# Kernel optimization log

Hardware: AMD Instinct MI355X
Metric: run time of the kernel (lower is better)

Reference implementation:

```python
import jax, jax.numpy as jnp
import numpy as np

N_NODES = 100000
N_USERS = 50000
F_DIM = 256
H = 128
N_EDGES = 800000
BATCH = 4096
LN_EPS = 1e-5


def setup_inputs() -> dict:
    key = jax.random.key(0)
    ks = jax.random.split(key, 12)
    return {
        "node_features": jax.random.normal(ks[0], (N_NODES, F_DIM), dtype=jnp.float32),
        "adj_row": jax.random.randint(ks[1], (N_EDGES,), 0, N_NODES),
        "adj_col": jax.random.randint(ks[2], (N_EDGES,), 0, N_NODES),
        "adj_vals": jax.random.uniform(ks[3], (N_EDGES,), dtype=jnp.float32),
        "user_idx": jax.random.randint(ks[4], (BATCH,), 0, N_USERS),
        "item_idx": jax.random.randint(ks[5], (BATCH,), 0, N_NODES),
        "W_proj": jax.random.normal(ks[6], (H, F_DIM), dtype=jnp.float32) * 0.02,
        "b_proj": jnp.zeros((H,), jnp.float32),
        "W1": jax.random.normal(ks[7], (H, H), dtype=jnp.float32) * 0.02,
        "b1": jnp.zeros((H,), jnp.float32),
        "W2": jax.random.normal(ks[8], (H, H), dtype=jnp.float32) * 0.02,
        "b2": jnp.zeros((H,), jnp.float32),
        "ln_g": jnp.ones((H,), jnp.float32),
        "ln_b": jnp.zeros((H,), jnp.float32),
        "user_emb": jax.random.normal(ks[9], (N_USERS, H), dtype=jnp.float32) * 0.01,
        "item_id_emb": jax.random.normal(ks[10], (N_NODES, H), dtype=jnp.float32) * 0.01,
        "user_bias": jnp.zeros((N_USERS, 1), jnp.float32),
        "item_bias": jnp.zeros((N_NODES, 1), jnp.float32),
        "global_bias": jnp.zeros((1,), jnp.float32),
    }


def _spmm(row, col, vals, x):
    # sparse COO adj @ x : gather neighbor rows, scale, scatter-add into dest rows
    return jax.ops.segment_sum(vals[:, None] * x[col], row, num_segments=x.shape[0])


def _layernorm(h, g, b):
    mu = jnp.mean(h, axis=-1, keepdims=True)
    var = jnp.mean(jnp.square(h - mu), axis=-1, keepdims=True)
    return (h - mu) * jax.lax.rsqrt(var + LN_EPS) * g + b


def reference(node_features, adj_row, adj_col, adj_vals, user_idx, item_idx,
              W_proj, b_proj, W1, b1, W2, b2, ln_g, ln_b,
              user_emb, item_id_emb, user_bias, item_bias, global_bias):
    # compute_item_embeddings (dropout is identity at eval)
    h = node_features @ W_proj.T + b_proj          # [N, H]
    residual = h
    for W, b in ((W1, b1), (W2, b2)):
        h = _spmm(adj_row, adj_col, adj_vals, h)   # sparse adj @ h
        h = h @ W.T + b
        h = jax.nn.relu(h)
        h = _layernorm(h, ln_g, ln_b)
    item_emb = h + residual + item_id_emb          # [N, H]

    # score(user_idx, item_idx, item_emb)
    u = user_emb[user_idx]                          # [B, H]
    i = item_emb[item_idx]                          # [B, H]
    bu = user_bias[user_idx, 0]
    bi = item_bias[item_idx, 0]
    return global_bias[0] + bu + bi + jnp.sum(u * i, axis=-1)  # [B]
```

## Files before the change

kernel.cpp:

```cpp
#include <hip/hip_runtime.h>

#define N_NODES 100000
#define N_USERS 50000
#define F_DIM 256
#define H 128
#define N_EDGES 800000
#define BATCH 4096
#define LN_EPS 1e-5f

typedef __attribute__((ext_vector_type(8))) short short8_t;
typedef __attribute__((ext_vector_type(8))) __bf16 bf16x8;
typedef __attribute__((ext_vector_type(4))) float f32x4;

__device__ inline unsigned short f2bf(float f) {
    unsigned int u = __builtin_bit_cast(unsigned int, f);
    unsigned int r = (u + 0x7fffu + ((u >> 16) & 1u)) >> 16;
    return (unsigned short)r;
}
__device__ inline float bf_lo(unsigned int u) {
    unsigned int x = u << 16; return __builtin_bit_cast(float, x);
}
__device__ inline float bf_hi(unsigned int u) {
    unsigned int x = u & 0xFFFF0000u; return __builtin_bit_cast(float, x);
}

__device__ inline bf16x8 cvt8(const float4 a0, const float4 a1) {
    short8_t af;
    af[0] = (short)f2bf(a0.x); af[1] = (short)f2bf(a0.y);
    af[2] = (short)f2bf(a0.z); af[3] = (short)f2bf(a0.w);
    af[4] = (short)f2bf(a1.x); af[5] = (short)f2bf(a1.y);
    af[6] = (short)f2bf(a1.z); af[7] = (short)f2bf(a1.w);
    return __builtin_bit_cast(bf16x8, af);
}

__global__ void pack_all_kernel(const float* __restrict__ Wp_, const float* __restrict__ W1_,
                                const float* __restrict__ W2_, short* __restrict__ oP,
                                short* __restrict__ o1, short* __restrict__ o2) {
    int idx = blockIdx.x * 256 + threadIdx.x;
    const float* W; short* o; int K; int local;
    if (idx < 32768)      { W = Wp_; o = oP; K = 256; local = idx; }
    else if (idx < 49152) { W = W1_; o = o1; K = 128; local = idx - 32768; }
    else                  { W = W2_; o = o2; K = 128; local = idx - 49152; }
    int i    = local & 7;
    int lane = (local >> 3) & 63;
    int c    = (local >> 9) & 7;
    int ks   = local >> 12;
    int j = c * 16 + (lane & 15);
    int k = ks * 32 + (lane >> 4) * 8 + i;
    o[local] = (short)f2bf(W[j * K + k]);
}

__global__ void zero_ints_kernel(int* __restrict__ p, int n) {
    int i = blockIdx.x * 256 + threadIdx.x;
    if (i < n) p[i] = 0;
}

__global__ void count_edges_kernel(const int* __restrict__ row, int* __restrict__ counts) {
    int e = blockIdx.x * 256 + threadIdx.x;
    if (e < N_EDGES) atomicAdd(&counts[row[e]], 1);
}

__global__ void scan_pass1_kernel(const int* __restrict__ counts, int* __restrict__ out,
                                  int* __restrict__ blockSums, int n) {
    __shared__ int lds[256];
    int b = blockIdx.x;
    int t = threadIdx.x;
    int base = b * 1024 + t * 4;
    int v0 = (base + 0 < n) ? counts[base + 0] : 0;
    int v1 = (base + 1 < n) ? counts[base + 1] : 0;
    int v2 = (base + 2 < n) ? counts[base + 2] : 0;
    int v3 = (base + 3 < n) ? counts[base + 3] : 0;
    int tsum = v0 + v1 + v2 + v3;
    lds[t] = tsum;
    __syncthreads();
    for (int off = 1; off < 256; off <<= 1) {
        int x = 0;
        if (t >= off) x = lds[t - off];
        __syncthreads();
        lds[t] += x;
        __syncthreads();
    }
    int excl = (t > 0) ? lds[t - 1] : 0;
    if (t == 255) blockSums[b] = lds[255];
    int e0 = excl, e1 = e0 + v0, e2 = e1 + v1, e3 = e2 + v2;
    if (base + 0 < n) out[base + 0] = e0;
    if (base + 1 < n) out[base + 1] = e1;
    if (base + 2 < n) out[base + 2] = e2;
    if (base + 3 < n) out[base + 3] = e3;
}

__global__ void scan_pass2_kernel(int* __restrict__ blockSums, int nb) {
    __shared__ int lds[128];
    int t = threadIdx.x;
    int v = (t < nb) ? blockSums[t] : 0;
    lds[t] = v;
    __syncthreads();
    for (int off = 1; off < 128; off <<= 1) {
        int x = (t >= off) ? lds[t - off] : 0;
        __syncthreads();
        lds[t] += x;
        __syncthreads();
    }
    if (t < nb) blockSums[t] = lds[t] - v;
}

__global__ void scan_pass3_kernel(int* __restrict__ row_start, int* __restrict__ cursor,
                                  const int* __restrict__ blockSums, int n) {
    int b = blockIdx.x;
    int t = threadIdx.x;
    int base = b * 1024 + t * 4;
    int add = blockSums[b];
    #pragma unroll
    for (int k = 0; k < 4; ++k) {
        int i = base + k;
        if (i < n) {
            int rs = row_start[i] + add;
            row_start[i] = rs;
            cursor[i] = rs;
        }
    }
}

__global__ void scatter_edges_kernel(const int* __restrict__ row, const int* __restrict__ col,
                                     const float* __restrict__ vals, int* __restrict__ cursor,
                                     int* __restrict__ ecol, float* __restrict__ evals) {
    int e = blockIdx.x * 256 + threadIdx.x;
    if (e >= N_EDGES) return;
    int r = row[e];
    int pos = atomicAdd(&cursor[r], 1);
    ecol[pos] = col[e];
    evals[pos] = vals[e];
}

__global__ __launch_bounds__(256) void proj_mfma_kernel(
        const float* __restrict__ A, const short* __restrict__ Bp,
        const float* __restrict__ bias, unsigned short* __restrict__ out) {
    const int tid  = threadIdx.x;
    const int lane = tid & 63;
    const int wt = blockIdx.x * 8 + (tid >> 6) * 2;
    if (wt >= N_NODES / 16) return;
    const int lrow = lane & 15;
    const int lk   = lane >> 4;

    const short8_t* Bv = (const short8_t*)Bp;
    f32x4 acc0[8], acc1[8];
    #pragma unroll
    for (int c = 0; c < 8; ++c) { acc0[c] = (f32x4)(0.f); acc1[c] = (f32x4)(0.f); }

    const float* Ar0 = A + (size_t)(wt * 16 + lrow) * F_DIM + lk * 8;
    const float* Ar1 = Ar0 + 16 * F_DIM;
    #pragma unroll 2
    for (int ks = 0; ks < 8; ++ks) {
        const float4* a0p = (const float4*)(Ar0 + ks * 32);
        const float4* a1p = (const float4*)(Ar1 + ks * 32);
        bf16x8 av0 = cvt8(a0p[0], a0p[1]);
        bf16x8 av1 = cvt8(a1p[0], a1p[1]);
        const short8_t* bp = Bv + (size_t)(ks * 8) * 64 + lane;
        #pragma unroll
        for (int c = 0; c < 8; ++c) {
            bf16x8 bv = __builtin_bit_cast(bf16x8, bp[c * 64]);
            acc0[c] = __builtin_amdgcn_mfma_f32_16x16x32_bf16(av0, bv, acc0[c], 0, 0, 0);
            acc1[c] = __builtin_amdgcn_mfma_f32_16x16x32_bf16(av1, bv, acc1[c], 0, 0, 0);
        }
    }
    #pragma unroll
    for (int c = 0; c < 8; ++c) {
        float bj = bias[c * 16 + lrow];
        const int or0 = wt * 16 + lk * 4;
        #pragma unroll
        for (int r = 0; r < 4; ++r) {
            out[(size_t)(or0 + r) * H + c * 16 + lrow] = f2bf(acc0[c][r] + bj);
            out[(size_t)(or0 + 16 + r) * H + c * 16 + lrow] = f2bf(acc1[c][r] + bj);
        }
    }
}

__global__ __launch_bounds__(256) void spmm_bf16_kernel(
        const unsigned short* __restrict__ hin, unsigned short* __restrict__ hout,
        const int* __restrict__ row_start, const int* __restrict__ ecol,
        const float* __restrict__ evals) {
    const int wave = threadIdx.x >> 6;
    const int lane = threadIdx.x & 63;
    const int row = blockIdx.x * 4 + wave;
    if (row >= N_NODES) return;
    const int s = row_start[row];
    const int e = (row + 1 < N_NODES) ? row_start[row + 1] : N_EDGES;
    const unsigned int* h32 = (const unsigned int*)hin;

    float ax0 = 0.f, ay0 = 0.f, ax1 = 0.f, ay1 = 0.f;
    float ax2 = 0.f, ay2 = 0.f, ax3 = 0.f, ay3 = 0.f;
    int p = s;
    for (; p + 4 <= e; p += 4) {
        int c0 = ecol[p + 0], c1 = ecol[p + 1], c2 = ecol[p + 2], c3 = ecol[p + 3];
        float v0 = evals[p + 0], v1 = evals[p + 1], v2 = evals[p + 2], v3 = evals[p + 3];
        unsigned int b0 = h32[(size_t)c0 * 64 + lane];
        unsigned int b1 = h32[(size_t)c1 * 64 + lane];
        unsigned int b2 = h32[(size_t)c2 * 64 + lane];
        unsigned int b3 = h32[(size_t)c3 * 64 + lane];
        ax0 += v0 * bf_lo(b0); ay0 += v0 * bf_hi(b0);
        ax1 += v1 * bf_lo(b1); ay1 += v1 * bf_hi(b1);
        ax2 += v2 * bf_lo(b2); ay2 += v2 * bf_hi(b2);
        ax3 += v3 * bf_lo(b3); ay3 += v3 * bf_hi(b3);
    }
    for (; p < e; ++p) {
        int c = ecol[p];
        float vv = evals[p];
        unsigned int hb = h32[(size_t)c * 64 + lane];
        ax0 += vv * bf_lo(hb); ay0 += vv * bf_hi(hb);
    }
    float ax = (ax0 + ax1) + (ax2 + ax3);
    float ay = (ay0 + ay1) + (ay2 + ay3);
    unsigned int w = (unsigned int)f2bf(ax) | ((unsigned int)f2bf(ay) << 16);
    ((unsigned int*)hout)[(size_t)row * 64 + lane] = w;
}

__device__ inline void mlp_epilogue(f32x4* acc, const float* __restrict__ bias,
                                    const float* __restrict__ g, const float* __restrict__ beta,
                                    unsigned short* __restrict__ out,
                                    int row0, int lrow, int lk) {
    float s1[4] = {0.f, 0.f, 0.f, 0.f};
    float s2[4] = {0.f, 0.f, 0.f, 0.f};
    #pragma unroll
    for (int c = 0; c < 8; ++c) {
        float bj = bias[c * 16 + lrow];
        #pragma unroll
        for (int r = 0; r < 4; ++r) {
            float x = fmaxf(acc[c][r] + bj, 0.f);
            acc[c][r] = x;
            s1[r] += x;
            s2[r] += x * x;
        }
    }
    #pragma unroll
    for (int r = 0; r < 4; ++r) {
        #pragma unroll
        for (int off = 1; off < 16; off <<= 1) {
            s1[r] += __shfl_xor(s1[r], off);
            s2[r] += __shfl_xor(s2[r], off);
        }
    }
    float mu[4], rr[4];
    #pragma unroll
    for (int r = 0; r < 4; ++r) {
        mu[r] = s1[r] * (1.f / 128.f);
        float var = s2[r] * (1.f / 128.f) - mu[r] * mu[r];
        rr[r] = rsqrtf(var + LN_EPS);
    }
    const int orow = row0 + lk * 4;
    #pragma unroll
    for (int c = 0; c < 8; ++c) {
        float gj  = g[c * 16 + lrow];
        float bj2 = beta[c * 16 + lrow];
        #pragma unroll
        for (int r = 0; r < 4; ++r)
            out[(size_t)(orow + r) * H + c * 16 + lrow] =
                f2bf((acc[c][r] - mu[r]) * rr[r] * gj + bj2);
    }
}

__global__ __launch_bounds__(256) void mlp_mfma_kernel(
        const unsigned short* __restrict__ X, const short* __restrict__ Bp,
        const float* __restrict__ bias, const float* __restrict__ g,
        const float* __restrict__ beta, unsigned short* __restrict__ out) {
    const int tid  = threadIdx.x;
    const int lane = tid & 63;
    const int wt = blockIdx.x * 8 + (tid >> 6) * 2;
    if (wt >= N_NODES / 16) return;
    const int lrow = lane & 15;
    const int lk   = lane >> 4;

    const short8_t* Bv = (const short8_t*)Bp;
    const short8_t* Xv0 = (const short8_t*)(X + (size_t)(wt * 16 + lrow) * H + lk * 8);
    const short8_t* Xv1 = (const short8_t*)(X + (size_t)((wt + 1) * 16 + lrow) * H + lk * 8);

    f32x4 acc0[8], acc1[8];
    #pragma unroll
    for (int c = 0; c < 8; ++c) { acc0[c] = (f32x4)(0.f); acc1[c] = (f32x4)(0.f); }

    #pragma unroll
    for (int ks = 0; ks < 4; ++ks) {
        bf16x8 av0 = __builtin_bit_cast(bf16x8, Xv0[ks * 4]);
        bf16x8 av1 = __builtin_bit_cast(bf16x8, Xv1[ks * 4]);
        const short8_t* bp = Bv + (size_t)(ks * 8) * 64 + lane;
        #pragma unroll
        for (int c = 0; c < 8; ++c) {
            bf16x8 bv = __builtin_bit_cast(bf16x8, bp[c * 64]);
            acc0[c] = __builtin_amdgcn_mfma_f32_16x16x32_bf16(av0, bv, acc0[c], 0, 0, 0);
            acc1[c] = __builtin_amdgcn_mfma_f32_16x16x32_bf16(av1, bv, acc1[c], 0, 0, 0);
        }
    }
    mlp_epilogue(acc0, bias, g, beta, out, wt * 16, lrow, lk);
    mlp_epilogue(acc1, bias, g, beta, out, (wt + 1) * 16, lrow, lk);
}

__global__ __launch_bounds__(256) void score_kernel(
        const unsigned short* __restrict__ hf, const unsigned short* __restrict__ h0,
        const float* __restrict__ iie, const float* __restrict__ uemb,
        const int* __restrict__ uidx, const int* __restrict__ iidx,
        const float* __restrict__ ubias, const float* __restrict__ ibias,
        const float* __restrict__ gbias, float* __restrict__ out) {
    const int wave = threadIdx.x >> 6;
    const int lane = threadIdx.x & 63;
    const int b = blockIdx.x * 4 + wave;
    if (b >= BATCH) return;
    const int u  = uidx[b];
    const int it = iidx[b];
    unsigned int b1 = ((const unsigned int*)hf)[(size_t)it * 64 + lane];
    unsigned int b2 = ((const unsigned int*)h0)[(size_t)it * 64 + lane];
    float2 x3 = ((const float2*)(iie + (size_t)it * H))[lane];
    float2 a  = ((const float2*)(uemb + (size_t)u * H))[lane];
    float p = a.x * (bf_lo(b1) + bf_lo(b2) + x3.x) +
              a.y * (bf_hi(b1) + bf_hi(b2) + x3.y);
    #pragma unroll
    for (int off = 32; off > 0; off >>= 1) p += __shfl_xor(p, off);
    if (lane == 0) out[b] = gbias[0] + ubias[u] + ibias[it] + p;
}


extern "C" void kernel_launch(void* const* d_in, const int* in_sizes, int n_in,
                              void* d_out, int out_size, void* d_ws, size_t ws_size,
                              hipStream_t stream) {
    const float* node_features = (const float*)d_in[0];
    const int*   adj_row       = (const int*)d_in[1];
    const int*   adj_col       = (const int*)d_in[2];
    const float* adj_vals      = (const float*)d_in[3];
    const int*   user_idx      = (const int*)d_in[4];
    const int*   item_idx      = (const int*)d_in[5];
    const float* W_proj        = (const float*)d_in[6];
    const float* b_proj        = (const float*)d_in[7];
    const float* W1            = (const float*)d_in[8];
    const float* b1            = (const float*)d_in[9];
    const float* W2            = (const float*)d_in[10];
    const float* b2            = (const float*)d_in[11];
    const float* ln_g          = (const float*)d_in[12];
    const float* ln_b          = (const float*)d_in[13];
    const float* user_emb      = (const float*)d_in[14];
    const float* item_id_emb   = (const float*)d_in[15];
    const float* user_bias     = (const float*)d_in[16];
    const float* item_bias     = (const float*)d_in[17];
    const float* global_bias   = (const float*)d_in[18];
    float* outp = (float*)d_out;

    char* ws = (char*)d_ws;
    size_t off = 0;
    auto alloc = [&](size_t bytes) -> void* {
        void* p = ws + off;
        off = (off + bytes + 255) & ~(size_t)255;
        return p;
    };

    unsigned short* h0 = (unsigned short*)alloc(sizeof(short) * (size_t)N_NODES * H);
    unsigned short* hA = (unsigned short*)alloc(sizeof(short) * (size_t)N_NODES * H);
    unsigned short* hB = (unsigned short*)alloc(sizeof(short) * (size_t)N_NODES * H);
    short* Wpp = (short*)alloc(sizeof(short) * F_DIM * H);
    short* W1p = (short*)alloc(sizeof(short) * H * H);
    short* W2p = (short*)alloc(sizeof(short) * H * H);
    int* counts    = (int*)alloc(sizeof(int) * N_NODES);
    int* row_start = (int*)alloc(sizeof(int) * N_NODES);
    int* cursor    = (int*)alloc(sizeof(int) * N_NODES);
    int* blockSums = (int*)alloc(sizeof(int) * 128);
    int* ecol      = (int*)alloc(sizeof(int) * N_EDGES);
    float* evals   = (float*)alloc(sizeof(float) * N_EDGES);

    const int NB = (N_NODES + 1023) / 1024;

    pack_all_kernel<<<256, 256, 0, stream>>>(W_proj, W1, W2, Wpp, W1p, W2p);

    zero_ints_kernel<<<(N_NODES + 255) / 256, 256, 0, stream>>>(counts, N_NODES);
    count_edges_kernel<<<N_EDGES / 256, 256, 0, stream>>>(adj_row, counts);
    scan_pass1_kernel<<<NB, 256, 0, stream>>>(counts, row_start, blockSums, N_NODES);
    scan_pass2_kernel<<<1, 128, 0, stream>>>(blockSums, NB);
    scan_pass3_kernel<<<NB, 256, 0, stream>>>(row_start, cursor, blockSums, N_NODES);
    scatter_edges_kernel<<<N_EDGES / 256, 256, 0, stream>>>(adj_row, adj_col, adj_vals,
                                                            cursor, ecol, evals);

    const int NT = N_NODES / 16;
    const int GT8 = (NT + 7) / 8;

    proj_mfma_kernel<<<GT8, 256, 0, stream>>>(node_features, Wpp, b_proj, h0);

    spmm_bf16_kernel<<<N_NODES / 4, 256, 0, stream>>>(h0, hA, row_start, ecol, evals);
    mlp_mfma_kernel<<<GT8, 256, 0, stream>>>(hA, W1p, b1, ln_g, ln_b, hB);

    spmm_bf16_kernel<<<N_NODES / 4, 256, 0, stream>>>(hB, hA, row_start, ecol, evals);
    mlp_mfma_kernel<<<GT8, 256, 0, stream>>>(hA, W2p, b2, ln_g, ln_b, hB);

    score_kernel<<<BATCH / 4, 256, 0, stream>>>(hB, h0, item_id_emb, user_emb,
                                                user_idx, item_idx, user_bias,
                                                item_bias, global_bias, outp);
}
```

Measured before the change: 487.2 us.

## Use one 16-row tile per wave with upfront A loads; shuffle-broadcast SpMM edges

The projection and MLP MFMA kernels now give each wave a single 16-row tile instead of two, and all A-operand loads are issued up front into registers. This doubles the number of waves to raise parallelism and memory-level overlap. The SpMM kernel loads up to 64 edge columns and values per row with one coalesced wave-wide load and broadcasts them by lane shuffle, replacing the scalar per-edge index loads; rows with more than 64 edges fall back to a tail loop. The cost is more register pressure from the preloaded A values and more redundant loads of B.

```diff
diff --git a/kernel.cpp b/kernel.cpp
--- a/kernel.cpp
+++ b/kernel.cpp
@@ -137,41 +137,42 @@
         const float* __restrict__ bias, unsigned short* __restrict__ out) {
     const int tid  = threadIdx.x;
     const int lane = tid & 63;
-    const int wt = blockIdx.x * 8 + (tid >> 6) * 2;
-    if (wt >= N_NODES / 16) return;
+    const int tile = blockIdx.x * 4 + (tid >> 6);
+    if (tile >= N_NODES / 16) return;
+    const int row0 = tile * 16;
     const int lrow = lane & 15;
     const int lk   = lane >> 4;
 
+    const float4* Ap = (const float4*)(A + (size_t)(row0 + lrow) * F_DIM + lk * 8);
+    float4 a[16];
+    #pragma unroll
+    for (int ks = 0; ks < 8; ++ks) {
+        a[2 * ks]     = Ap[ks * 8];
+        a[2 * ks + 1] = Ap[ks * 8 + 1];
+    }
+
     const short8_t* Bv = (const short8_t*)Bp;
-    f32x4 acc0[8], acc1[8];
-    #pragma unroll
-    for (int c = 0; c < 8; ++c) { acc0[c] = (f32x4)(0.f); acc1[c] = (f32x4)(0.f); }
-
-    const float* Ar0 = A + (size_t)(wt * 16 + lrow) * F_DIM + lk * 8;
-    const float* Ar1 = Ar0 + 16 * F_DIM;
-    #pragma unroll 2
+    f32x4 acc[8];
+    #pragma unroll
+    for (int c = 0; c < 8; ++c) acc[c] = (f32x4)(0.f);
+
+    #pragma unroll
     for (int ks = 0; ks < 8; ++ks) {
-        const float4* a0p = (const float4*)(Ar0 + ks * 32);
-        const float4* a1p = (const float4*)(Ar1 + ks * 32);
-        bf16x8 av0 = cvt8(a0p[0], a0p[1]);
-        bf16x8 av1 = cvt8(a1p[0], a1p[1]);
+        bf16x8 av = cvt8(a[2 * ks], a[2 * ks + 1]);
         const short8_t* bp = Bv + (size_t)(ks * 8) * 64 + lane;
         #pragma unroll
         for (int c = 0; c < 8; ++c) {
             bf16x8 bv = __builtin_bit_cast(bf16x8, bp[c * 64]);
-            acc0[c] = __builtin_amdgcn_mfma_f32_16x16x32_bf16(av0, bv, acc0[c], 0, 0, 0);
-            acc1[c] = __builtin_amdgcn_mfma_f32_16x16x32_bf16(av1, bv, acc1[c], 0, 0, 0);
+            acc[c] = __builtin_amdgcn_mfma_f32_16x16x32_bf16(av, bv, acc[c], 0, 0, 0);
         }
     }
+    const int orow = row0 + lk * 4;
     #pragma unroll
     for (int c = 0; c < 8; ++c) {
         float bj = bias[c * 16 + lrow];
-        const int or0 = wt * 16 + lk * 4;
-        #pragma unroll
-        for (int r = 0; r < 4; ++r) {
-            out[(size_t)(or0 + r) * H + c * 16 + lrow] = f2bf(acc0[c][r] + bj);
-            out[(size_t)(or0 + 16 + r) * H + c * 16 + lrow] = f2bf(acc1[c][r] + bj);
-        }
+        #pragma unroll
+        for (int r = 0; r < 4; ++r)
+            out[(size_t)(orow + r) * H + c * 16 + lrow] = f2bf(acc[c][r] + bj);
     }
 }
 
@@ -185,14 +186,24 @@
     if (row >= N_NODES) return;
     const int s = row_start[row];
     const int e = (row + 1 < N_NODES) ? row_start[row + 1] : N_EDGES;
+    const int deg = e - s;
     const unsigned int* h32 = (const unsigned int*)hin;
+
+    int mi = s + lane;
+    int idxm = (mi < N_EDGES) ? mi : (N_EDGES - 1);
+    int   c_all = ecol[idxm];
+    float v_all = (mi < e) ? evals[idxm] : 0.f;
 
     float ax0 = 0.f, ay0 = 0.f, ax1 = 0.f, ay1 = 0.f;
     float ax2 = 0.f, ay2 = 0.f, ax3 = 0.f, ay3 = 0.f;
-    int p = s;
-    for (; p + 4 <= e; p += 4) {
-        int c0 = ecol[p + 0], c1 = ecol[p + 1], c2 = ecol[p + 2], c3 = ecol[p + 3];
-        float v0 = evals[p + 0], v1 = evals[p + 1], v2 = evals[p + 2], v3 = evals[p + 3];
+
+    const int dmain = (deg < 64) ? deg : 64;
+    #pragma unroll 2
+    for (int p = 0; p < dmain; p += 4) {
+        int   c0 = __shfl(c_all, p + 0); float v0 = __shfl(v_all, p + 0);
+        int   c1 = __shfl(c_all, p + 1); float v1 = __shfl(v_all, p + 1);
+        int   c2 = __shfl(c_all, p + 2); float v2 = __shfl(v_all, p + 2);
+        int   c3 = __shfl(c_all, p + 3); float v3 = __shfl(v_all, p + 3);
         unsigned int b0 = h32[(size_t)c0 * 64 + lane];
         unsigned int b1 = h32[(size_t)c1 * 64 + lane];
         unsigned int b2 = h32[(size_t)c2 * 64 + lane];
@@ -202,7 +213,7 @@
         ax2 += v2 * bf_lo(b2); ay2 += v2 * bf_hi(b2);
         ax3 += v3 * bf_lo(b3); ay3 += v3 * bf_hi(b3);
     }
-    for (; p < e; ++p) {
+    for (int p = s + 64; p < e; ++p) {
         int c = ecol[p];
         float vv = evals[p];
         unsigned int hb = h32[(size_t)c * 64 + lane];
@@ -264,33 +275,33 @@
         const float* __restrict__ beta, unsigned short* __restrict__ out) {
     const int tid  = threadIdx.x;
     const int lane = tid & 63;
-    const int wt = blockIdx.x * 8 + (tid >> 6) * 2;
-    if (wt >= N_NODES / 16) return;
+    const int tile = blockIdx.x * 4 + (tid >> 6);
+    if (tile >= N_NODES / 16) return;
+    const int row0 = tile * 16;
     const int lrow = lane & 15;
     const int lk   = lane >> 4;
 
+    const short8_t* Xv = (const short8_t*)(X + (size_t)(row0 + lrow) * H + lk * 8);
+    short8_t x[4];
+    #pragma unroll
+    for (int ks = 0; ks < 4; ++ks) x[ks] = Xv[ks * 4];
+
     const short8_t* Bv = (const short8_t*)Bp;
-    const short8_t* Xv0 = (const short8_t*)(X + (size_t)(wt * 16 + lrow) * H + lk * 8);
-    const short8_t* Xv1 = (const short8_t*)(X + (size_t)((wt + 1) * 16 + lrow) * H + lk * 8);
-
-    f32x4 acc0[8], acc1[8];
-    #pragma unroll
-    for (int c = 0; c < 8; ++c) { acc0[c] = (f32x4)(0.f); acc1[c] = (f32x4)(0.f); }
+    f32x4 acc[8];
+    #pragma unroll
+    for (int c = 0; c < 8; ++c) acc[c] = (f32x4)(0.f);
 
     #pragma unroll
     for (int ks = 0; ks < 4; ++ks) {
-        bf16x8 av0 = __builtin_bit_cast(bf16x8, Xv0[ks * 4]);
-        bf16x8 av1 = __builtin_bit_cast(bf16x8, Xv1[ks * 4]);
+        bf16x8 av = __builtin_bit_cast(bf16x8, x[ks]);
         const short8_t* bp = Bv + (size_t)(ks * 8) * 64 + lane;
         #pragma unroll
         for (int c = 0; c < 8; ++c) {
             bf16x8 bv = __builtin_bit_cast(bf16x8, bp[c * 64]);
-            acc0[c] = __builtin_amdgcn_mfma_f32_16x16x32_bf16(av0, bv, acc0[c], 0, 0, 0);
-            acc1[c] = __builtin_amdgcn_mfma_f32_16x16x32_bf16(av1, bv, acc1[c], 0, 0, 0);
+            acc[c] = __builtin_amdgcn_mfma_f32_16x16x32_bf16(av, bv, acc[c], 0, 0, 0);
         }
     }
-    mlp_epilogue(acc0, bias, g, beta, out, wt * 16, lrow, lk);
-    mlp_epilogue(acc1, bias, g, beta, out, (wt + 1) * 16, lrow, lk);
+    mlp_epilogue(acc, bias, g, beta, out, row0, lrow, lk);
 }
 
 __global__ __launch_bounds__(256) void score_kernel(
@@ -375,15 +386,15 @@
                                                             cursor, ecol, evals);
 
     const int NT = N_NODES / 16;
-    const int GT8 = (NT + 7) / 8;
-
-    proj_mfma_kernel<<<GT8, 256, 0, stream>>>(node_features, Wpp, b_proj, h0);
+    const int GT4 = (NT + 3) / 4;
+
+    proj_mfma_kernel<<<GT4, 256, 0, stream>>>(node_features, Wpp, b_proj, h0);
 
     spmm_bf16_kernel<<<N_NODES / 4, 256, 0, stream>>>(h0, hA, row_start, ecol, evals);
-    mlp_mfma_kernel<<<GT8, 256, 0, stream>>>(hA, W1p, b1, ln_g, ln_b, hB);
+    mlp_mfma_kernel<<<GT4, 256, 0, stream>>>(hA, W1p, b1, ln_g, ln_b, hB);
 
     spmm_bf16_kernel<<<N_NODES / 4, 256, 0, stream>>>(hB, hA, row_start, ecol, evals);
-    mlp_mfma_kernel<<<GT8, 256, 0, stream>>>(hA, W2p, b2, ln_g, ln_b, hB);
+    mlp_mfma_kernel<<<GT4, 256, 0, stream>>>(hA, W2p, b2, ln_g, ln_b, hB);
 
     score_kernel<<<BATCH / 4, 256, 0, stream>>>(hB, h0, item_id_emb, user_emb,
                                                 user_idx, item_idx, user_bias,
```

Measured after the change: 445.2 us. -8.6%, faster.
